# Kernel tuning notes

Measured on AMD Instinct MI355X. Metric: run time of the kernel, lower is better.

Reference implementation:

```python
import jax, jax.numpy as jnp
import numpy as np

HIDDEN = 1024

def setup_inputs() -> dict:
    key = jax.random.key(0)
    ks = jax.random.split(key, 7)
    B, S, H = 4, 4096, HIDDEN
    scale = 1.0 / np.sqrt(H)
    return {
        "x": jax.random.normal(ks[0], (B, S, H), dtype=jnp.float32),
        "Wq": jax.random.normal(ks[1], (H, H), dtype=jnp.float32) * scale,
        "bq": jnp.zeros((H,), dtype=jnp.float32),
        "Wk": jax.random.normal(ks[2], (H, H), dtype=jnp.float32) * scale,
        "bk": jnp.zeros((H,), dtype=jnp.float32),
        "Wv": jax.random.normal(ks[3], (H, H), dtype=jnp.float32) * scale,
        "bv": jnp.zeros((H,), dtype=jnp.float32),
    }

def reference(x, Wq, bq, Wk, bk, Wv, bv):
    # Linear layers: y = x @ W^T + b (torch nn.Linear convention)
    q = jnp.einsum('bsh,oh->bso', x, Wq) + bq
    k = jnp.einsum('bsh,oh->bso', x, Wk) + bk
    v = jnp.einsum('bsh,oh->bso', x, Wv) + bv
    # NOTE: source applies NO 1/sqrt(d) scaling — faithful reproduction.
    scores = jnp.einsum('bqh,bkh->bqk', q, k)  # [B,S,S]
    attn = jax.nn.softmax(scores, axis=-1)
    return jnp.einsum('bqk,bkh->bqh', attn, v)
```

## Files before the change

kernel.cpp:

```cpp
#include <hip/hip_runtime.h>
#include <math.h>
#include <type_traits>


typedef unsigned short u16;
typedef _Float16 f16x8 __attribute__((ext_vector_type(8)));
typedef __bf16 bf16x8 __attribute__((ext_vector_type(8)));
typedef float f32x4 __attribute__((ext_vector_type(4)));
struct __align__(8) u16x4 { u16 x, y, z, w; };

__device__ __forceinline__ u16 f2bf(float f) {
    unsigned u = __builtin_bit_cast(unsigned, f);
    u += 0x7fffu + ((u >> 16) & 1u);
    return (u16)(u >> 16);
}
__device__ __forceinline__ u16 f2h(float f) {
    _Float16 h = (_Float16)f;
    return __builtin_bit_cast(u16, h);
}
__device__ __forceinline__ float h2f(u16 h) {
    return (float)__builtin_bit_cast(_Float16, h);
}

#define MF16(a, b, c) __builtin_amdgcn_mfma_f32_16x16x32_f16( \
    __builtin_bit_cast(f16x8, a), __builtin_bit_cast(f16x8, b), c, 0, 0, 0)
#define MBF16(a, b, c) __builtin_amdgcn_mfma_f32_16x16x32_bf16(a, b, c, 0, 0, 0)

#define SLOT_E  (4u * 1024 * 1024)
#define BBLK_E  (16u * 1024 * 1024)

__global__ __launch_bounds__(512, 4) void gemm_projqk(
    const u16* __restrict__ xh, const u16* __restrict__ xl,
    const u16* __restrict__ Wq, const u16* __restrict__ Wk,
    const float* __restrict__ bq, const float* __restrict__ bk,
    u16* __restrict__ qout, u16* __restrict__ kout)
{
    __shared__ char lds[4 * 8192];
    const int K = 1024, lda = 1024, ldb = 1024, ldc = 1024, nbx = 8;

    const int cpx = (int)gridDim.x >> 3;
    const int raw = blockIdx.x;
    const int swz = (raw & 7) * cpx + (raw >> 3);
    const int bm = (swz / nbx) * 128, bn = (swz % nbx) * 128;

    const int t = threadIdx.x;
    const int w = t >> 6, lane = t & 63;
    const int qksel = w >> 2;
    const int wl = w & 3;
    const int wr = wl >> 1, wc = wl & 1;
    const int r16 = lane & 15, g = lane >> 4;

    f32x4 acc[4][4];
#pragma unroll
    for (int i = 0; i < 4; ++i)
#pragma unroll
        for (int j = 0; j < 4; ++j) acc[i][j] = (f32x4)0.0f;

    for (int k0 = 0; k0 < K; k0 += 32) {
#pragma unroll
        for (int i = 0; i < 4; ++i) {
            const int ch = w * 4 + i;
            const int tt = ch >> 3, sub = ch & 7;
            const int s = sub * 64 + lane;
            const int row = s >> 2;
            const int kg = (s & 3) ^ ((row >> 1) & 3);
            const u16* P = (tt == 0) ? xh : (tt == 1) ? xl : (tt == 2) ? Wq : Wk;
            const int rbase = (tt < 2) ? bm : bn;
            const int ld = (tt < 2) ? lda : ldb;
            __builtin_amdgcn_global_load_lds(
                (const __attribute__((address_space(1))) void*)
                    (P + (size_t)(rbase + row) * ld + k0 + kg * 8),
                (__attribute__((address_space(3))) void*)(lds + ch * 1024),
                16, 0, 0);
        }
        __syncthreads();

        bf16x8 fa[2][4], fb[4];
#pragma unroll
        for (int i = 0; i < 4; ++i) {
            const int ra = wr * 64 + i * 16 + r16;
            const int oa = ra * 64 + ((g ^ ((ra >> 1) & 3)) << 4);
            fa[0][i] = *(const bf16x8*)(lds + oa);
            fa[1][i] = *(const bf16x8*)(lds + 8192 + oa);
            const int rbw = wc * 64 + i * 16 + r16;
            const int ob = rbw * 64 + ((g ^ ((rbw >> 1) & 3)) << 4);
            fb[i] = *(const bf16x8*)(lds + (2 + qksel) * 8192 + ob);
        }
#pragma unroll
        for (int i = 0; i < 4; ++i)
#pragma unroll
            for (int j = 0; j < 4; ++j) {
                acc[i][j] = MF16(fa[0][i], fb[j], acc[i][j]);
                acc[i][j] = MF16(fa[1][i], fb[j], acc[i][j]);
            }
        __syncthreads();
    }

    u16* Cout = qksel ? kout : qout;
    const float* bias = qksel ? bk : bq;
#pragma unroll
    for (int j = 0; j < 4; ++j) {
        const int gc = bn + wc * 64 + j * 16 + r16;
        const float bv = bias[gc];
#pragma unroll
        for (int i = 0; i < 4; ++i) {
            const int gr = bm + wr * 64 + i * 16 + g * 4;
#pragma unroll
            for (int r = 0; r < 4; ++r) {
                const int grr = gr + r;
                const size_t bb = (size_t)(grr >> 12) * BBLK_E;
                Cout[bb + (size_t)(grr & 4095) * ldc + gc] = f2h(acc[i][j][r] + bv);
            }
        }
    }
}

#define GEMM_PARAMS const u16* __restrict__ A0, const u16* __restrict__ B0, \
    int K, int lda, int ldb, const float* __restrict__ bias, \
    float* __restrict__ Cf, u16* __restrict__ Ch, \
    int ldc, int nbx, unsigned long long zsA, unsigned long long zsB, \
    unsigned long long zsC

template<int VAR>
__device__ __forceinline__ void gemm8_body(GEMM_PARAMS)
{
    __shared__ char lds[2 * 24576];

    const int cpx = (int)gridDim.x >> 3;
    const int raw = blockIdx.x;
    const int swz = (raw & 7) * cpx + (raw >> 3);
    const int bm = (swz / nbx) * 128, bn = (swz % nbx) * 256;

    const unsigned long long z = blockIdx.z;
    A0 += z * zsA;
    B0 += z * zsB;

    const int t = threadIdx.x;
    const int w = t >> 6, lane = t & 63;
    const int wr = w >> 2, wc = w & 3;
    const int r16 = lane & 15, g = lane >> 4;

    f32x4 acc[4][4];
#pragma unroll
    for (int i = 0; i < 4; ++i)
#pragma unroll
        for (int j = 0; j < 4; ++j) acc[i][j] = (f32x4)0.0f;

    auto STAGE = [&](auto BO, int k0) {
#pragma unroll
        for (int i = 0; i < 3; ++i) {
            constexpr int bufo = decltype(BO)::value;
            const int ch = w * 3 + i;
            const int isB = (ch >= 8);
            const int cb = isB ? (ch - 8) : ch;
            const int row = cb * 16 + (lane >> 2);
            const int kg = (lane & 3) ^ ((row >> 1) & 3);
            const u16* P = isB ? B0 : A0;
            const int rbase = isB ? bn : bm;
            const int ld = isB ? ldb : lda;
            __builtin_amdgcn_global_load_lds(
                (const __attribute__((address_space(1))) void*)
                    (P + (size_t)(rbase + row) * ld + k0 + kg * 8),
                (__attribute__((address_space(3))) void*)
                    (lds + bufo + (isB ? 8192 : 0) + cb * 1024),
                16, 0, 0);
        }
    };

    bf16x8 fa[4], fb[4];
    auto FRAGS = [&](auto BO) {
        constexpr int bufo = decltype(BO)::value;
#pragma unroll
        for (int i = 0; i < 4; ++i) {
            const int ra = wr * 64 + i * 16 + r16;
            fa[i] = *(const bf16x8*)(lds + bufo + ra * 64 + ((g ^ ((ra >> 1) & 3)) << 4));
            const int rb = wc * 64 + i * 16 + r16;
            fb[i] = *(const bf16x8*)(lds + bufo + 8192 + rb * 64 + ((g ^ ((rb >> 1) & 3)) << 4));
        }
    };
    auto MM = [&]() {
#pragma unroll
        for (int i = 0; i < 4; ++i)
#pragma unroll
            for (int j = 0; j < 4; ++j) {
                if constexpr (VAR == 3) acc[i][j] = MBF16(fa[i], fb[j], acc[i][j]);
                else                    acc[i][j] = MF16(fa[i], fb[j], acc[i][j]);
            }
    };

    std::integral_constant<int, 0> c0;
    std::integral_constant<int, 24576> c1;

    const int nk = K >> 5;
    STAGE(c0, 0);
    STAGE(c1, 1 << 5);
    for (int tt = 0; tt + 2 < nk; tt += 2) {
        asm volatile("s_waitcnt vmcnt(3)\n\ts_barrier" ::: "memory");
        FRAGS(c0);
        asm volatile("s_waitcnt lgkmcnt(0)\n\ts_barrier" ::: "memory");
        STAGE(c0, (tt + 2) << 5);
        MM();
        asm volatile("s_waitcnt vmcnt(3)\n\ts_barrier" ::: "memory");
        FRAGS(c1);
        asm volatile("s_waitcnt lgkmcnt(0)\n\ts_barrier" ::: "memory");
        STAGE(c1, (tt + 3) << 5);
        MM();
    }
    asm volatile("s_waitcnt vmcnt(3)\n\ts_barrier" ::: "memory");
    FRAGS(c0);
    MM();
    asm volatile("s_waitcnt vmcnt(0)\n\ts_barrier" ::: "memory");
    FRAGS(c1);
    MM();

#pragma unroll
    for (int j = 0; j < 4; ++j) {
        const int gc = bn + wc * 64 + j * 16 + r16;
        const float bv = bias ? bias[gc] : 0.0f;
#pragma unroll
        for (int i = 0; i < 4; ++i) {
            const int gr = bm + wr * 64 + i * 16 + g * 4;
#pragma unroll
            for (int r = 0; r < 4; ++r) {
                const float val = acc[i][j][r] + bv;
                const int grr = gr + r;
                if constexpr (VAR == 1) {
                    Ch[(size_t)gc * ldc + grr] = f2bf(val);
                } else {
                    Cf[z * zsC + (size_t)grr * ldc + gc] = val;
                }
            }
        }
    }
}

__global__ __launch_bounds__(512, 4) void gemm_projv(GEMM_PARAMS) { gemm8_body<1>(A0,B0,K,lda,ldb,bias,Cf,Ch,ldc,nbx,zsA,zsB,zsC); }
__global__ __launch_bounds__(512, 4) void gemm_scores(GEMM_PARAMS){ gemm8_body<2>(A0,B0,K,lda,ldb,bias,Cf,Ch,ldc,nbx,zsA,zsB,zsC); }
__global__ __launch_bounds__(512, 4) void gemm_pv(GEMM_PARAMS)    { gemm8_body<3>(A0,B0,K,lda,ldb,bias,Cf,Ch,ldc,nbx,zsA,zsB,zsC); }

__global__ __launch_bounds__(256) void split_h(
    const float* __restrict__ in, u16* __restrict__ hi, u16* __restrict__ lo, int n4)
{
    const int i = blockIdx.x * 256 + threadIdx.x;
    if (i >= n4) return;
    const float4 v = ((const float4*)in)[i];
    u16x4 h, l;
    h.x = f2h(v.x); l.x = f2h(v.x - h2f(h.x));
    h.y = f2h(v.y); l.y = f2h(v.y - h2f(h.y));
    h.z = f2h(v.z); l.z = f2h(v.z - h2f(h.z));
    h.w = f2h(v.w); l.w = f2h(v.w - h2f(h.w));
    ((u16x4*)hi)[i] = h;
    ((u16x4*)lo)[i] = l;
}

__global__ __launch_bounds__(256) void softmax4096(
    const float* __restrict__ S, u16* __restrict__ P)
{
    const float* p = S + (size_t)blockIdx.x * 4096;
    u16* q = P + (size_t)blockIdx.x * 4096;
    const int t = threadIdx.x;
    const int wave = t >> 6, lane = t & 63;
    __shared__ float red[8];

    float4 v[4];
    float mx = -INFINITY;
#pragma unroll
    for (int i = 0; i < 4; ++i) {
        v[i] = ((const float4*)p)[i * 256 + t];
        mx = fmaxf(mx, fmaxf(fmaxf(v[i].x, v[i].y), fmaxf(v[i].z, v[i].w)));
    }
#pragma unroll
    for (int o = 32; o > 0; o >>= 1) mx = fmaxf(mx, __shfl_xor(mx, o));
    if (lane == 0) red[wave] = mx;
    __syncthreads();
    mx = fmaxf(fmaxf(red[0], red[1]), fmaxf(red[2], red[3]));

    float sum = 0.f;
#pragma unroll
    for (int i = 0; i < 4; ++i) {
        v[i].x = __expf(v[i].x - mx);
        v[i].y = __expf(v[i].y - mx);
        v[i].z = __expf(v[i].z - mx);
        v[i].w = __expf(v[i].w - mx);
        sum += (v[i].x + v[i].y) + (v[i].z + v[i].w);
    }
#pragma unroll
    for (int o = 32; o > 0; o >>= 1) sum += __shfl_xor(sum, o);
    if (lane == 0) red[4 + wave] = sum;
    __syncthreads();
    sum = (red[4] + red[5]) + (red[6] + red[7]);

    const float inv = 1.0f / sum;
#pragma unroll
    for (int i = 0; i < 4; ++i) {
        u16x4 u;
        u.x = f2bf(v[i].x * inv); u.y = f2bf(v[i].y * inv);
        u.z = f2bf(v[i].z * inv); u.w = f2bf(v[i].w * inv);
        ((u16x4*)q)[i * 256 + t] = u;
    }
}

extern "C" void kernel_launch(void* const* d_in, const int* in_sizes, int n_in,
                              void* d_out, int out_size, void* d_ws, size_t ws_size,
                              hipStream_t stream)
{
    const float* x  = (const float*)d_in[0];
    const float* Wq = (const float*)d_in[1];
    const float* bq = (const float*)d_in[2];
    const float* Wk = (const float*)d_in[3];
    const float* bk = (const float*)d_in[4];
    const float* Wv = (const float*)d_in[5];
    const float* bv = (const float*)d_in[6];
    float* out = (float*)d_out;

    const int B = 4, S = 4096, H = 1024;
    const size_t MB = 1u << 20;
    if (ws_size < 256 * MB) return;
    char* wsp = (char*)d_ws;

    u16* xh = (u16*)(wsp);
    u16* xl = (u16*)(wsp + 32 * MB);
    float* sc = (float*)(wsp);
    u16* qk = (u16*)(wsp + 64 * MB);
    u16* vT = (u16*)(wsp + 192 * MB);
    u16* Wqh = (u16*)(wsp + 224 * MB), *Wql = (u16*)(wsp + 226 * MB);
    u16* Wkh = (u16*)(wsp + 228 * MB), *Wkl = (u16*)(wsp + 230 * MB);
    u16* Wvh = (u16*)(wsp + 232 * MB), *Wvl = (u16*)(wsp + 234 * MB);

    const dim3 blk(256);
    float* nulf = nullptr;

    hipLaunchKernelGGL(split_h, dim3(B * S * H / 4 / 256), blk, 0, stream, x, xh, xl, B * S * H / 4);
    hipLaunchKernelGGL(split_h, dim3(H * H / 4 / 256), blk, 0, stream, Wq, Wqh, Wql, H * H / 4);
    hipLaunchKernelGGL(split_h, dim3(H * H / 4 / 256), blk, 0, stream, Wk, Wkh, Wkl, H * H / 4);
    hipLaunchKernelGGL(split_h, dim3(H * H / 4 / 256), blk, 0, stream, Wv, Wvh, Wvl, H * H / 4);

    hipLaunchKernelGGL(gemm_projqk, dim3(1024), dim3(512), 0, stream,
        xh, xl, Wqh, Wkh, bq, bk,
        qk + 0 * SLOT_E, qk + 1 * SLOT_E);
    hipLaunchKernelGGL(gemm_projv, dim3(512), dim3(512), 0, stream,
        xh, Wvh, H, H, H, bv,
        nulf, vT, B * S, 4, 0ull, 0ull, 0ull);

    for (int b = 0; b < B; ++b) {
        const u16* qb = qk + (size_t)b * BBLK_E;
        hipLaunchKernelGGL(gemm_scores, dim3(512), dim3(512), 0, stream,
            qb, qb + SLOT_E,
            H, H, H, (const float*)nullptr,
            sc, (u16*)nullptr, S, 16, 0ull, 0ull, 0ull);
        hipLaunchKernelGGL(softmax4096, dim3(S), blk, 0, stream,
            sc, qk + (size_t)b * BBLK_E);
    }

    hipLaunchKernelGGL(gemm_pv, dim3(128, 1, 4), dim3(512), 0, stream,
        qk, vT,
        S, S, B * S, (const float*)nullptr,
        out, (u16*)nullptr, H, 4,
        (unsigned long long)BBLK_E, 4096ull, (unsigned long long)S * H);
}
```

Before: 563.1 us.

## Double-buffer QK projection GEMM and triple-buffer PV GEMM loads

Replaces the single-buffered QK projection loop, which synchronised twice per k-step, with a two-stage LDS ping-pong pipeline that uses async global-to-LDS loads and vmcnt waits. The generic GEMM gains a DEPTH template parameter, and the PV GEMM now uses a three-buffer pipeline so loads are issued further ahead of use. The goal is to hide global load latency behind MFMA work. In exchange, LDS use per block grows (64KB for projqk, 72KB for pv), which may cut the number of resident blocks per CU.

```diff
diff --git a/kernel.cpp b/kernel.cpp
--- a/kernel.cpp
+++ b/kernel.cpp
@@ -35,7 +35,7 @@
     const float* __restrict__ bq, const float* __restrict__ bk,
     u16* __restrict__ qout, u16* __restrict__ kout)
 {
-    __shared__ char lds[4 * 8192];
+    __shared__ char lds[2 * 32768];
     const int K = 1024, lda = 1024, ldb = 1024, ldc = 1024, nbx = 8;
 
     const int cpx = (int)gridDim.x >> 3;
@@ -56,9 +56,10 @@
 #pragma unroll
         for (int j = 0; j < 4; ++j) acc[i][j] = (f32x4)0.0f;
 
-    for (int k0 = 0; k0 < K; k0 += 32) {
+    auto STAGE = [&](auto BO, int k0) {
 #pragma unroll
         for (int i = 0; i < 4; ++i) {
+            constexpr int bufo = decltype(BO)::value;
             const int ch = w * 4 + i;
             const int tt = ch >> 3, sub = ch & 7;
             const int s = sub * 64 + lane;
@@ -70,22 +71,26 @@
             __builtin_amdgcn_global_load_lds(
                 (const __attribute__((address_space(1))) void*)
                     (P + (size_t)(rbase + row) * ld + k0 + kg * 8),
-                (__attribute__((address_space(3))) void*)(lds + ch * 1024),
+                (__attribute__((address_space(3))) void*)(lds + bufo + ch * 1024),
                 16, 0, 0);
         }
-        __syncthreads();
-
-        bf16x8 fa[2][4], fb[4];
+    };
+
+    bf16x8 fa[2][4], fb[4];
+    auto FRAGS = [&](auto BO) {
+        constexpr int bufo = decltype(BO)::value;
 #pragma unroll
         for (int i = 0; i < 4; ++i) {
             const int ra = wr * 64 + i * 16 + r16;
             const int oa = ra * 64 + ((g ^ ((ra >> 1) & 3)) << 4);
-            fa[0][i] = *(const bf16x8*)(lds + oa);
-            fa[1][i] = *(const bf16x8*)(lds + 8192 + oa);
+            fa[0][i] = *(const bf16x8*)(lds + bufo + oa);
+            fa[1][i] = *(const bf16x8*)(lds + bufo + 8192 + oa);
             const int rbw = wc * 64 + i * 16 + r16;
             const int ob = rbw * 64 + ((g ^ ((rbw >> 1) & 3)) << 4);
-            fb[i] = *(const bf16x8*)(lds + (2 + qksel) * 8192 + ob);
-        }
+            fb[i] = *(const bf16x8*)(lds + bufo + (2 + qksel) * 8192 + ob);
+        }
+    };
+    auto MM = [&]() {
 #pragma unroll
         for (int i = 0; i < 4; ++i)
 #pragma unroll
@@ -93,8 +98,32 @@
                 acc[i][j] = MF16(fa[0][i], fb[j], acc[i][j]);
                 acc[i][j] = MF16(fa[1][i], fb[j], acc[i][j]);
             }
-        __syncthreads();
-    }
+    };
+
+    std::integral_constant<int, 0> c0;
+    std::integral_constant<int, 32768> c1;
+
+    const int nk = K >> 5;
+    STAGE(c0, 0);
+    STAGE(c1, 1 << 5);
+    for (int tt = 0; tt + 2 < nk; tt += 2) {
+        asm volatile("s_waitcnt vmcnt(4)\n\ts_barrier" ::: "memory");
+        FRAGS(c0);
+        asm volatile("s_waitcnt lgkmcnt(0)\n\ts_barrier" ::: "memory");
+        STAGE(c0, (tt + 2) << 5);
+        MM();
+        asm volatile("s_waitcnt vmcnt(4)\n\ts_barrier" ::: "memory");
+        FRAGS(c1);
+        asm volatile("s_waitcnt lgkmcnt(0)\n\ts_barrier" ::: "memory");
+        STAGE(c1, (tt + 3) << 5);
+        MM();
+    }
+    asm volatile("s_waitcnt vmcnt(4)\n\ts_barrier" ::: "memory");
+    FRAGS(c0);
+    MM();
+    asm volatile("s_waitcnt vmcnt(0)\n\ts_barrier" ::: "memory");
+    FRAGS(c1);
+    MM();
 
     u16* Cout = qksel ? kout : qout;
     const float* bias = qksel ? bk : bq;
@@ -121,10 +150,10 @@
     int ldc, int nbx, unsigned long long zsA, unsigned long long zsB, \
     unsigned long long zsC
 
-template<int VAR>
+template<int VAR, int DEPTH>
 __device__ __forceinline__ void gemm8_body(GEMM_PARAMS)
 {
-    __shared__ char lds[2 * 24576];
+    __shared__ char lds[(DEPTH + 1) * 24576];
 
     const int cpx = (int)gridDim.x >> 3;
     const int raw = blockIdx.x;
@@ -190,28 +219,59 @@
 
     std::integral_constant<int, 0> c0;
     std::integral_constant<int, 24576> c1;
+    std::integral_constant<int, 49152> c2;
 
     const int nk = K >> 5;
-    STAGE(c0, 0);
-    STAGE(c1, 1 << 5);
-    for (int tt = 0; tt + 2 < nk; tt += 2) {
+
+    if constexpr (DEPTH == 1) {
+        STAGE(c0, 0);
+        STAGE(c1, 1 << 5);
+        for (int tt = 0; tt + 2 < nk; tt += 2) {
+            asm volatile("s_waitcnt vmcnt(3)\n\ts_barrier" ::: "memory");
+            FRAGS(c0);
+            asm volatile("s_waitcnt lgkmcnt(0)\n\ts_barrier" ::: "memory");
+            STAGE(c0, (tt + 2) << 5);
+            MM();
+            asm volatile("s_waitcnt vmcnt(3)\n\ts_barrier" ::: "memory");
+            FRAGS(c1);
+            asm volatile("s_waitcnt lgkmcnt(0)\n\ts_barrier" ::: "memory");
+            STAGE(c1, (tt + 3) << 5);
+            MM();
+        }
         asm volatile("s_waitcnt vmcnt(3)\n\ts_barrier" ::: "memory");
         FRAGS(c0);
-        asm volatile("s_waitcnt lgkmcnt(0)\n\ts_barrier" ::: "memory");
-        STAGE(c0, (tt + 2) << 5);
-        MM();
+        MM();
+        asm volatile("s_waitcnt vmcnt(0)\n\ts_barrier" ::: "memory");
+        FRAGS(c1);
+        MM();
+    } else {
+        STAGE(c0, 0);
+        STAGE(c1, 1 << 5);
+        STAGE(c2, 2 << 5);
+        for (int tt = 0; tt + 4 < nk; tt += 3) {
+            asm volatile("s_waitcnt vmcnt(6)\n\ts_barrier" ::: "memory");
+            FRAGS(c0);
+            asm volatile("s_waitcnt lgkmcnt(0)\n\ts_barrier" ::: "memory");
+            STAGE(c0, (tt + 3) << 5);
+            MM();
+            asm volatile("s_waitcnt vmcnt(6)\n\ts_barrier" ::: "memory");
+            FRAGS(c1);
+            asm volatile("s_waitcnt lgkmcnt(0)\n\ts_barrier" ::: "memory");
+            STAGE(c1, (tt + 4) << 5);
+            MM();
+            asm volatile("s_waitcnt vmcnt(6)\n\ts_barrier" ::: "memory");
+            FRAGS(c2);
+            asm volatile("s_waitcnt lgkmcnt(0)\n\ts_barrier" ::: "memory");
+            if (tt + 5 < nk) STAGE(c2, (tt + 5) << 5);
+            MM();
+        }
         asm volatile("s_waitcnt vmcnt(3)\n\ts_barrier" ::: "memory");
+        FRAGS(c0);
+        MM();
+        asm volatile("s_waitcnt vmcnt(0)\n\ts_barrier" ::: "memory");
         FRAGS(c1);
-        asm volatile("s_waitcnt lgkmcnt(0)\n\ts_barrier" ::: "memory");
-        STAGE(c1, (tt + 3) << 5);
-        MM();
-    }
-    asm volatile("s_waitcnt vmcnt(3)\n\ts_barrier" ::: "memory");
-    FRAGS(c0);
-    MM();
-    asm volatile("s_waitcnt vmcnt(0)\n\ts_barrier" ::: "memory");
-    FRAGS(c1);
-    MM();
+        MM();
+    }
 
 #pragma unroll
     for (int j = 0; j < 4; ++j) {
@@ -234,9 +294,9 @@
     }
 }
 
-__global__ __launch_bounds__(512, 4) void gemm_projv(GEMM_PARAMS) { gemm8_body<1>(A0,B0,K,lda,ldb,bias,Cf,Ch,ldc,nbx,zsA,zsB,zsC); }
-__global__ __launch_bounds__(512, 4) void gemm_scores(GEMM_PARAMS){ gemm8_body<2>(A0,B0,K,lda,ldb,bias,Cf,Ch,ldc,nbx,zsA,zsB,zsC); }
-__global__ __launch_bounds__(512, 4) void gemm_pv(GEMM_PARAMS)    { gemm8_body<3>(A0,B0,K,lda,ldb,bias,Cf,Ch,ldc,nbx,zsA,zsB,zsC); }
+__global__ __launch_bounds__(512, 4) void gemm_projv(GEMM_PARAMS) { gemm8_body<1, 1>(A0,B0,K,lda,ldb,bias,Cf,Ch,ldc,nbx,zsA,zsB,zsC); }
+__global__ __launch_bounds__(512, 4) void gemm_scores(GEMM_PARAMS){ gemm8_body<2, 1>(A0,B0,K,lda,ldb,bias,Cf,Ch,ldc,nbx,zsA,zsB,zsC); }
+__global__ __launch_bounds__(512, 4) void gemm_pv(GEMM_PARAMS)    { gemm8_body<3, 2>(A0,B0,K,lda,ldb,bias,Cf,Ch,ldc,nbx,zsA,zsB,zsC); }
 
 __global__ __launch_bounds__(256) void split_h(
     const float* __restrict__ in, u16* __restrict__ hi, u16* __restrict__ lo, int n4)
```

Result: slower. 998.1 us (+77.3%).

## Use 128x128 tile GEMM variant for scores and PV to double block count

Applied to the files above, without the earlier changes.

Adds a separate GEMM body with 128x128 output tiles (each wave computes 64x32), a smaller LDS footprint, and two async loads per thread per stage. Scores and PV now use it, which doubles their grid sizes, while the old 256-wide kernel is kept only for the V projection. The aim is more blocks per CU and better load balance across the device, at the cost of lower operand reuse per tile and more global traffic.

```diff
diff --git a/kernel.cpp b/kernel.cpp
--- a/kernel.cpp
+++ b/kernel.cpp
@@ -182,10 +182,8 @@
 #pragma unroll
         for (int i = 0; i < 4; ++i)
 #pragma unroll
-            for (int j = 0; j < 4; ++j) {
-                if constexpr (VAR == 3) acc[i][j] = MBF16(fa[i], fb[j], acc[i][j]);
-                else                    acc[i][j] = MF16(fa[i], fb[j], acc[i][j]);
-            }
+            for (int j = 0; j < 4; ++j)
+                acc[i][j] = MF16(fa[i], fb[j], acc[i][j]);
     };
 
     std::integral_constant<int, 0> c0;
@@ -224,19 +222,125 @@
             for (int r = 0; r < 4; ++r) {
                 const float val = acc[i][j][r] + bv;
                 const int grr = gr + r;
-                if constexpr (VAR == 1) {
-                    Ch[(size_t)gc * ldc + grr] = f2bf(val);
-                } else {
-                    Cf[z * zsC + (size_t)grr * ldc + gc] = val;
-                }
+                Ch[(size_t)gc * ldc + grr] = f2bf(val);
             }
         }
     }
 }
 
+template<int VAR>
+__device__ __forceinline__ void gemm8s_body(GEMM_PARAMS)
+{
+    __shared__ char lds[2 * 16384];
+
+    const int cpx = (int)gridDim.x >> 3;
+    const int raw = blockIdx.x;
+    const int swz = (raw & 7) * cpx + (raw >> 3);
+    const int bm = (swz / nbx) * 128, bn = (swz % nbx) * 128;
+
+    const unsigned long long z = blockIdx.z;
+    A0 += z * zsA;
+    B0 += z * zsB;
+
+    const int t = threadIdx.x;
+    const int w = t >> 6, lane = t & 63;
+    const int wr = w >> 2, wc = w & 3;
+    const int r16 = lane & 15, g = lane >> 4;
+
+    f32x4 acc[4][2];
+#pragma unroll
+    for (int i = 0; i < 4; ++i)
+#pragma unroll
+        for (int j = 0; j < 2; ++j) acc[i][j] = (f32x4)0.0f;
+
+    auto STAGE = [&](auto BO, int k0) {
+#pragma unroll
+        for (int i = 0; i < 2; ++i) {
+            constexpr int bufo = decltype(BO)::value;
+            const int ch = w * 2 + i;
+            const int isB = (ch >= 8);
+            const int cb = ch & 7;
+            const int row = cb * 16 + (lane >> 2);
+            const int kg = (lane & 3) ^ ((row >> 1) & 3);
+            const u16* P = isB ? B0 : A0;
+            const int rbase = isB ? bn : bm;
+            const int ld = isB ? ldb : lda;
+            __builtin_amdgcn_global_load_lds(
+                (const __attribute__((address_space(1))) void*)
+                    (P + (size_t)(rbase + row) * ld + k0 + kg * 8),
+                (__attribute__((address_space(3))) void*)
+                    (lds + bufo + (isB ? 8192 : 0) + cb * 1024),
+                16, 0, 0);
+        }
+    };
+
+    bf16x8 fa[4], fb[2];
+    auto FRAGS = [&](auto BO) {
+        constexpr int bufo = decltype(BO)::value;
+#pragma unroll
+        for (int i = 0; i < 4; ++i) {
+            const int ra = wr * 64 + i * 16 + r16;
+            fa[i] = *(const bf16x8*)(lds + bufo + ra * 64 + ((g ^ ((ra >> 1) & 3)) << 4));
+        }
+#pragma unroll
+        for (int j = 0; j < 2; ++j) {
+            const int rb = wc * 32 + j * 16 + r16;
+            fb[j] = *(const bf16x8*)(lds + bufo + 8192 + rb * 64 + ((g ^ ((rb >> 1) & 3)) << 4));
+        }
+    };
+    auto MM = [&]() {
+#pragma unroll
+        for (int i = 0; i < 4; ++i)
+#pragma unroll
+            for (int j = 0; j < 2; ++j) {
+                if constexpr (VAR == 3) acc[i][j] = MBF16(fa[i], fb[j], acc[i][j]);
+                else                    acc[i][j] = MF16(fa[i], fb[j], acc[i][j]);
+            }
+    };
+
+    std::integral_constant<int, 0> c0;
+    std::integral_constant<int, 16384> c1;
+
+    const int nk = K >> 5;
+    STAGE(c0, 0);
+    STAGE(c1, 1 << 5);
+    for (int tt = 0; tt + 2 < nk; tt += 2) {
+        asm volatile("s_waitcnt vmcnt(2)\n\ts_barrier" ::: "memory");
+        FRAGS(c0);
+        asm volatile("s_waitcnt lgkmcnt(0)\n\ts_barrier" ::: "memory");
+        STAGE(c0, (tt + 2) << 5);
+        MM();
+        asm volatile("s_waitcnt vmcnt(2)\n\ts_barrier" ::: "memory");
+        FRAGS(c1);
+        asm volatile("s_waitcnt lgkmcnt(0)\n\ts_barrier" ::: "memory");
+        STAGE(c1, (tt + 3) << 5);
+        MM();
+    }
+    asm volatile("s_waitcnt vmcnt(2)\n\ts_barrier" ::: "memory");
+    FRAGS(c0);
+    MM();
+    asm volatile("s_waitcnt vmcnt(0)\n\ts_barrier" ::: "memory");
+    FRAGS(c1);
+    MM();
+
+#pragma unroll
+    for (int j = 0; j < 2; ++j) {
+        const int gc = bn + wc * 32 + j * 16 + r16;
+#pragma unroll
+        for (int i = 0; i < 4; ++i) {
+            const int gr = bm + wr * 64 + i * 16 + g * 4;
+#pragma unroll
+            for (int r = 0; r < 4; ++r) {
+                const int grr = gr + r;
+                Cf[z * zsC + (size_t)grr * ldc + gc] = acc[i][j][r];
+            }
+        }
+    }
+}
+
 __global__ __launch_bounds__(512, 4) void gemm_projv(GEMM_PARAMS) { gemm8_body<1>(A0,B0,K,lda,ldb,bias,Cf,Ch,ldc,nbx,zsA,zsB,zsC); }
-__global__ __launch_bounds__(512, 4) void gemm_scores(GEMM_PARAMS){ gemm8_body<2>(A0,B0,K,lda,ldb,bias,Cf,Ch,ldc,nbx,zsA,zsB,zsC); }
-__global__ __launch_bounds__(512, 4) void gemm_pv(GEMM_PARAMS)    { gemm8_body<3>(A0,B0,K,lda,ldb,bias,Cf,Ch,ldc,nbx,zsA,zsB,zsC); }
+__global__ __launch_bounds__(512, 4) void gemm_scores(GEMM_PARAMS){ gemm8s_body<2>(A0,B0,K,lda,ldb,bias,Cf,Ch,ldc,nbx,zsA,zsB,zsC); }
+__global__ __launch_bounds__(512, 4) void gemm_pv(GEMM_PARAMS)    { gemm8s_body<3>(A0,B0,K,lda,ldb,bias,Cf,Ch,ldc,nbx,zsA,zsB,zsC); }
 
 __global__ __launch_bounds__(256) void split_h(
     const float* __restrict__ in, u16* __restrict__ hi, u16* __restrict__ lo, int n4)
@@ -344,17 +448,17 @@
 
     for (int b = 0; b < B; ++b) {
         const u16* qb = qk + (size_t)b * BBLK_E;
-        hipLaunchKernelGGL(gemm_scores, dim3(512), dim3(512), 0, stream,
+        hipLaunchKernelGGL(gemm_scores, dim3(1024), dim3(512), 0, stream,
             qb, qb + SLOT_E,
             H, H, H, (const float*)nullptr,
-            sc, (u16*)nullptr, S, 16, 0ull, 0ull, 0ull);
+            sc, (u16*)nullptr, S, 32, 0ull, 0ull, 0ull);
         hipLaunchKernelGGL(softmax4096, dim3(S), blk, 0, stream,
             sc, qk + (size_t)b * BBLK_E);
     }
 
-    hipLaunchKernelGGL(gemm_pv, dim3(128, 1, 4), dim3(512), 0, stream,
+    hipLaunchKernelGGL(gemm_pv, dim3(256, 1, 4), dim3(512), 0, stream,
         qk, vT,
         S, S, B * S, (const float*)nullptr,
-        out, (u16*)nullptr, H, 4,
+        out, (u16*)nullptr, H, 8,
         (unsigned long long)BBLK_E, 4096ull, (unsigned long long)S * H);
 }
```

Measured after the change: 619.8 us. 10.1% more time.
